# Kernel optimization log

Measured on AMD Instinct MI355X. Metric: run time of the kernel, lower is better.

The kernel has to match this reference:

```python
import jax, jax.numpy as jnp
import numpy as np

B, S, E, H = 1, 2048, 512, 8
D = E // H
N = B * S
WIN_HALF = 32  # attention_window 64 -> +/-32
ALPHA = 0.1
LN_EPS = 1e-12
NEG_INF = -1e9


def _build_window_edges():
    # windowed graph: dst i attends to src j with |i-j| <= WIN_HALF, within each batch block
    i = np.arange(S)
    offs = np.arange(-WIN_HALF, WIN_HALF + 1)
    src = i[:, None] + offs[None, :]
    dst = np.broadcast_to(i[:, None], src.shape)
    valid = (src >= 0) & (src < S)
    src, dst = src[valid], dst[valid]
    srcs, dsts = [], []
    for b in range(B):
        srcs.append(src + b * S)
        dsts.append(dst + b * S)
    return (np.concatenate(srcs).astype(np.int32),
            np.concatenate(dsts).astype(np.int32))


def setup_inputs() -> dict:
    key = jax.random.key(0)
    ks = jax.random.split(key, 12)
    sc = 1.0 / np.sqrt(E)
    src_np, dst_np = _build_window_edges()
    return {
        "hidden_states": jax.random.normal(ks[0], (B, S, E), dtype=jnp.float32),
        "attention_mask": jnp.zeros((B, S), dtype=jnp.float32),
        "edge_src": jnp.asarray(src_np),
        "edge_dst": jnp.asarray(dst_np),
        "Wq": jax.random.normal(ks[1], (E, E), dtype=jnp.float32) * sc,
        "bq": jnp.zeros((E,), dtype=jnp.float32),
        "Wk": jax.random.normal(ks[2], (E, E), dtype=jnp.float32) * sc,
        "bk": jnp.zeros((E,), dtype=jnp.float32),
        "Wv": jax.random.normal(ks[3], (E, E), dtype=jnp.float32) * sc,
        "bv": jnp.zeros((E,), dtype=jnp.float32),
        "Wo": jax.random.normal(ks[4], (E, E), dtype=jnp.float32) * sc,
        "bo": jnp.zeros((E,), dtype=jnp.float32),
        "ln_g": jnp.ones((E,), dtype=jnp.float32),
        "ln_b": jnp.zeros((E,), dtype=jnp.float32),
    }


def reference(hidden_states, attention_mask, edge_src, edge_dst,
              Wq, bq, Wk, bk, Wv, bv, Wo, bo, ln_g, ln_b):
    x = hidden_states  # (B,S,E); node ordering n = b*S + s (matches torch reshape)
    q = ((x @ Wq + bq) / jnp.sqrt(jnp.asarray(D, x.dtype))).reshape(N, H, D)
    k = (x @ Wk + bk).reshape(N, H, D)
    v = (x @ Wv + bv).reshape(N, H, D)

    mask = (attention_mask >= 0).reshape(N)  # bool per node

    # u_dot_v('k','q','score'): per-edge, per-head dot product
    score = jnp.einsum('ehd,ehd->eh', k[edge_src], q[edge_dst])  # (Eg,H)
    score = jnp.where(mask[edge_src][:, None], score, NEG_INF)

    # edge_softmax over incoming edges of each destination node
    smax = jax.ops.segment_max(score, edge_dst, num_segments=N)
    p = jnp.exp(score - smax[edge_dst])
    denom = jax.ops.segment_sum(p, edge_dst, num_segments=N)
    p = p / denom[edge_dst]  # (Eg,H)

    # 5 diffusion steps: h <- A h, blended with residual v (dropout off in eval)
    h = v
    for _ in range(5):
        m = h[edge_src] * p[:, :, None]                      # u_mul_e
        h = jax.ops.segment_sum(m, edge_dst, num_segments=N)  # sum('m','h')
        h = (1.0 - ALPHA) * h + ALPHA * v

    attn = h.reshape(B, S, E)

    # DiffuserSelfOutput: dense -> residual add -> LayerNorm
    y = attn @ Wo + bo + hidden_states
    mu = y.mean(-1, keepdims=True)
    var = ((y - mu) ** 2).mean(-1, keepdims=True)
    out = (y - mu) * jax.lax.rsqrt(var + LN_EPS) * ln_g + ln_b
    return out
```

## Files before the change

kernel.cpp:

```cpp
#include <hip/hip_runtime.h>
#include <math.h>

#define S_LEN 2048
#define E_DIM 512
#define NE (S_LEN * E_DIM)
#define H_NUM 8
#define WH 32
#define NOFF 65
#define PROW (H_NUM * NOFF)
#define PN (S_LEN * PROW)

typedef float f32x4 __attribute__((ext_vector_type(4)));
typedef short short8 __attribute__((ext_vector_type(8)));

__device__ __forceinline__ unsigned short f2bf(float f) {
    union { float f; unsigned u; } cv; cv.f = f;
    unsigned u = cv.u;
    u += 0x7fffu + ((u >> 16) & 1u);
    return (unsigned short)(u >> 16);
}
__device__ __forceinline__ unsigned pk2(float x, float y) {
    return (unsigned)f2bf(x) | ((unsigned)f2bf(y) << 16);
}

__device__ __forceinline__ void mfma_gemm_f32(
    const float* __restrict__ A, const float* __restrict__ W,
    const float* __restrict__ bias, float* __restrict__ C,
    float scale, int m0, int n0)
{
    __shared__ unsigned short As[64 * 40];
    __shared__ unsigned short Bs[64 * 40];
    const int tid = threadIdx.x;
    const int lane = tid & 63, wave = tid >> 6;
    const int quad = lane >> 4, l16 = lane & 15;
    const int wr = (wave >> 1) * 32, wc = (wave & 1) * 32;
    const int ar = tid >> 2, ac = (tid & 3) * 8;
    const int bn = tid & 63, bk0 = (tid >> 6) * 8;

    f32x4 acc00 = {0.f,0.f,0.f,0.f}, acc01 = acc00, acc10 = acc00, acc11 = acc00;

    for (int kk = 0; kk < E_DIM; kk += 32) {
        float4 a0 = *(const float4*)(A + (size_t)(m0 + ar) * E_DIM + kk + ac);
        float4 a1 = *(const float4*)(A + (size_t)(m0 + ar) * E_DIM + kk + ac + 4);
        float b[8];
#pragma unroll
        for (int j = 0; j < 8; ++j)
            b[j] = W[(size_t)(kk + bk0 + j) * E_DIM + n0 + bn];
        __syncthreads();
        uint4 ap; ap.x = pk2(a0.x, a0.y); ap.y = pk2(a0.z, a0.w);
        ap.z = pk2(a1.x, a1.y); ap.w = pk2(a1.z, a1.w);
        *(uint4*)(As + ar * 40 + ac) = ap;
        uint4 bp; bp.x = pk2(b[0], b[1]); bp.y = pk2(b[2], b[3]);
        bp.z = pk2(b[4], b[5]); bp.w = pk2(b[6], b[7]);
        *(uint4*)(Bs + bn * 40 + bk0) = bp;
        __syncthreads();
        short8 fa0 = *(const short8*)(As + (wr + l16) * 40 + quad * 8);
        short8 fa1 = *(const short8*)(As + (wr + 16 + l16) * 40 + quad * 8);
        short8 fb0 = *(const short8*)(Bs + (wc + l16) * 40 + quad * 8);
        short8 fb1 = *(const short8*)(Bs + (wc + 16 + l16) * 40 + quad * 8);
        acc00 = __builtin_amdgcn_mfma_f32_16x16x32_bf16(fa0, fb0, acc00, 0, 0, 0);
        acc01 = __builtin_amdgcn_mfma_f32_16x16x32_bf16(fa0, fb1, acc01, 0, 0, 0);
        acc10 = __builtin_amdgcn_mfma_f32_16x16x32_bf16(fa1, fb0, acc10, 0, 0, 0);
        acc11 = __builtin_amdgcn_mfma_f32_16x16x32_bf16(fa1, fb1, acc11, 0, 0, 0);
    }

#pragma unroll
    for (int mi = 0; mi < 2; ++mi) {
#pragma unroll
        for (int ni = 0; ni < 2; ++ni) {
            f32x4 a = (mi == 0) ? ((ni == 0) ? acc00 : acc01)
                                : ((ni == 0) ? acc10 : acc11);
            int n = n0 + wc + ni * 16 + l16;
            float bval = bias[n];
#pragma unroll
            for (int r = 0; r < 4; ++r) {
                int m = m0 + wr + mi * 16 + quad * 4 + r;
                C[(size_t)m * E_DIM + n] = (a[r] + bval) * scale;
            }
        }
    }
}

__global__ __launch_bounds__(256)
void qkv_gemm(const float* __restrict__ x,
              const float* __restrict__ Wq, const float* __restrict__ bq,
              const float* __restrict__ Wk, const float* __restrict__ bk,
              const float* __restrict__ Wv, const float* __restrict__ bv,
              float* __restrict__ q, float* __restrict__ k, float* __restrict__ v)
{
    const float* W; const float* b; float* o; float sc;
    if (blockIdx.z == 0)      { W = Wq; b = bq; o = q; sc = 0.125f; }
    else if (blockIdx.z == 1) { W = Wk; b = bk; o = k; sc = 1.0f; }
    else                      { W = Wv; b = bv; o = v; sc = 1.0f; }
    mfma_gemm_f32(x, W, b, o, sc, blockIdx.y * 64, blockIdx.x * 64);
}

#define SDN 32
__global__ __launch_bounds__(256)
void scores_kernel(const float* __restrict__ q, const float* __restrict__ k,
                   const float* __restrict__ amask, float* __restrict__ P)
{
    const int i0 = blockIdx.x * SDN;
    const int h  = blockIdx.y;
    const int tid = threadIdx.x;
    __shared__ float ks[96 * 68];
    __shared__ float am[96];
    __shared__ float sc[SDN * 66];
    __shared__ float smx[SDN], sidn[SDN];

    for (int e = tid; e < 96 * 16; e += 256) {
        int lr = e >> 4, c4 = e & 15;
        int j = i0 - WH + lr;
        int jc = min(max(j, 0), S_LEN - 1);
        *(float4*)(ks + lr * 68 + c4 * 4) =
            *(const float4*)(k + (size_t)jc * E_DIM + h * 64 + c4 * 4);
    }
    if (tid < 96) {
        int j = i0 - WH + tid;
        am[tid] = (j >= 0 && j < S_LEN) ? amask[j] : -1.0f;
    }

    const int dst = tid >> 3;
    const int og  = tid & 7;
    float4 qreg[16];
    {
        const float4* qrow = (const float4*)(q + (size_t)(i0 + dst) * E_DIM + h * 64);
#pragma unroll
        for (int t = 0; t < 16; ++t) qreg[t] = qrow[t];
    }
    __syncthreads();

    for (int off = og; off < NOFF; off += 8) {
        int j = i0 + dst + off - WH;
        float s;
        if (j < 0 || j >= S_LEN) {
            s = -INFINITY;
        } else {
            int lr = dst + off;
            const float4* kr = (const float4*)(ks + lr * 68);
            float acc = 0.f;
#pragma unroll
            for (int t = 0; t < 16; ++t) {
                float4 a = qreg[t], bb = kr[t];
                acc += a.x * bb.x + a.y * bb.y + a.z * bb.z + a.w * bb.w;
            }
            s = (am[lr] >= 0.f) ? acc : -1e9f;
        }
        sc[dst * 66 + off] = s;
    }
    __syncthreads();

    if (tid < SDN) {
        float mx = -INFINITY;
        for (int o = 0; o < NOFF; ++o) mx = fmaxf(mx, sc[tid * 66 + o]);
        float dn = 0.f;
        for (int o = 0; o < NOFF; ++o) dn += expf(sc[tid * 66 + o] - mx);
        smx[tid] = mx; sidn[tid] = 1.f / dn;
    }
    __syncthreads();

    for (int e = tid; e < SDN * NOFF; e += 256) {
        int d = e / NOFF, off = e - d * NOFF;
        float pv = expf(sc[d * 66 + off] - smx[d]) * sidn[d];
        P[(size_t)(i0 + d) * PROW + h * NOFF + off] = pv;
    }
}

__global__ __launch_bounds__(512)
void diffuse2(const float* __restrict__ hin, const float* __restrict__ v,
              const float* __restrict__ P, float* __restrict__ hout)
{
    const int i0 = blockIdx.x * 64;
    const int h  = blockIdx.y;
    const int tid = threadIdx.x;
    __shared__ float hs[192 * 64];
    __shared__ float h1[128 * 64];
    __shared__ float ps[128 * NOFF];

    for (int e = tid; e < 192 * 16; e += 512) {
        int lr = e >> 4, c4 = e & 15;
        int j = i0 - 64 + lr;
        int jc = min(max(j, 0), S_LEN - 1);
        *(float4*)(hs + lr * 64 + c4 * 4) =
            *(const float4*)(hin + (size_t)jc * E_DIM + h * 64 + c4 * 4);
    }
    for (int e = tid; e < 128 * NOFF; e += 512) {
        int mr = e / NOFF, o = e - mr * NOFF;
        int j = i0 - 32 + mr;
        int jc = min(max(j, 0), S_LEN - 1);
        ps[e] = P[(size_t)jc * PROW + h * NOFF + o];
    }
    __syncthreads();

    const int c4 = (tid & 15) * 4;
    const int g  = tid >> 4;
    const float4* h4 = (const float4*)hs;
    const int ci = tid & 15;

    {
        float4 a0 = {0,0,0,0}, a1 = a0, a2 = a0, a3 = a0;
        const int mb = g * 4;
        for (int lr = mb; lr < mb + 68; ++lr) {
            float4 hval = h4[lr * 16 + ci];
            int o0 = lr - mb;
            if ((unsigned)o0 <= 64u) {
                float p = ps[(mb + 0) * NOFF + o0];
                a0.x += p * hval.x; a0.y += p * hval.y; a0.z += p * hval.z; a0.w += p * hval.w;
            }
            int o1 = o0 - 1;
            if ((unsigned)o1 <= 64u) {
                float p = ps[(mb + 1) * NOFF + o1];
                a1.x += p * hval.x; a1.y += p * hval.y; a1.z += p * hval.z; a1.w += p * hval.w;
            }
            int o2 = o0 - 2;
            if ((unsigned)o2 <= 64u) {
                float p = ps[(mb + 2) * NOFF + o2];
                a2.x += p * hval.x; a2.y += p * hval.y; a2.z += p * hval.z; a2.w += p * hval.w;
            }
            int o3 = o0 - 3;
            if ((unsigned)o3 <= 64u) {
                float p = ps[(mb + 3) * NOFF + o3];
                a3.x += p * hval.x; a3.y += p * hval.y; a3.z += p * hval.z; a3.w += p * hval.w;
            }
        }
#pragma unroll
        for (int r = 0; r < 4; ++r) {
            float4 a = (r == 0) ? a0 : (r == 1) ? a1 : (r == 2) ? a2 : a3;
            int j = i0 - 32 + mb + r;
            int jc = min(max(j, 0), S_LEN - 1);
            float4 vv = *(const float4*)(v + (size_t)jc * E_DIM + h * 64 + c4);
            float4 o;
            o.x = 0.9f * a.x + 0.1f * vv.x;
            o.y = 0.9f * a.y + 0.1f * vv.y;
            o.z = 0.9f * a.z + 0.1f * vv.z;
            o.w = 0.9f * a.w + 0.1f * vv.w;
            *(float4*)(h1 + (mb + r) * 64 + c4) = o;
        }
    }
    __syncthreads();

    {
        const int ob = g * 2;
        const float4* m4 = (const float4*)h1;
        float4 a0 = {0,0,0,0}, a1 = a0;
        for (int lr = ob; lr < ob + 66; ++lr) {
            float4 hval = m4[lr * 16 + ci];
            int o0 = lr - ob;
            if ((unsigned)o0 <= 64u) {
                float p = ps[(ob + 32) * NOFF + o0];
                a0.x += p * hval.x; a0.y += p * hval.y; a0.z += p * hval.z; a0.w += p * hval.w;
            }
            int o1 = o0 - 1;
            if ((unsigned)o1 <= 64u) {
                float p = ps[(ob + 33) * NOFF + o1];
                a1.x += p * hval.x; a1.y += p * hval.y; a1.z += p * hval.z; a1.w += p * hval.w;
            }
        }
#pragma unroll
        for (int r = 0; r < 2; ++r) {
            float4 a = (r == 0) ? a0 : a1;
            size_t base = (size_t)(i0 + ob + r) * E_DIM + h * 64 + c4;
            float4 vv = *(const float4*)(v + base);
            float4 o;
            o.x = 0.9f * a.x + 0.1f * vv.x;
            o.y = 0.9f * a.y + 0.1f * vv.y;
            o.z = 0.9f * a.z + 0.1f * vv.z;
            o.w = 0.9f * a.w + 0.1f * vv.w;
            *(float4*)(hout + base) = o;
        }
    }
}

__global__ __launch_bounds__(256)
void diffuse1(const float* __restrict__ hin, const float* __restrict__ v,
              const float* __restrict__ P, float* __restrict__ hout)
{
    const int i0 = blockIdx.x * 32;
    const int h  = blockIdx.y;
    const int tid = threadIdx.x;
    __shared__ float hs[96 * 64];
    __shared__ float ps[32 * NOFF];

    for (int e = tid; e < 96 * 16; e += 256) {
        int lr = e >> 4, c4 = e & 15;
        int j = i0 - WH + lr;
        int jc = min(max(j, 0), S_LEN - 1);
        *(float4*)(hs + lr * 64 + c4 * 4) =
            *(const float4*)(hin + (size_t)jc * E_DIM + h * 64 + c4 * 4);
    }
    for (int e = tid; e < 32 * NOFF; e += 256) {
        int mr = e / NOFF, o = e - mr * NOFF;
        ps[e] = P[(size_t)(i0 + mr) * PROW + h * NOFF + o];
    }
    __syncthreads();

    const int c4 = (tid & 15) * 4;
    const int ci = tid & 15;
    const int g  = tid >> 4;
    const int ob = g * 2;
    const float4* h4 = (const float4*)hs;

    float4 a0 = {0,0,0,0}, a1 = a0;
    for (int lr = ob; lr < ob + 66; ++lr) {
        float4 hval = h4[lr * 16 + ci];
        int o0 = lr - ob;
        if ((unsigned)o0 <= 64u) {
            float p = ps[(ob + 0) * NOFF + o0];
            a0.x += p * hval.x; a0.y += p * hval.y; a0.z += p * hval.z; a0.w += p * hval.w;
        }
        int o1 = o0 - 1;
        if ((unsigned)o1 <= 64u) {
            float p = ps[(ob + 1) * NOFF + o1];
            a1.x += p * hval.x; a1.y += p * hval.y; a1.z += p * hval.z; a1.w += p * hval.w;
        }
    }
#pragma unroll
    for (int r = 0; r < 2; ++r) {
        float4 a = (r == 0) ? a0 : a1;
        size_t base = (size_t)(i0 + ob + r) * E_DIM + h * 64 + c4;
        float4 vv = *(const float4*)(v + base);
        float4 o;
        o.x = 0.9f * a.x + 0.1f * vv.x;
        o.y = 0.9f * a.y + 0.1f * vv.y;
        o.z = 0.9f * a.z + 0.1f * vv.z;
        o.w = 0.9f * a.w + 0.1f * vv.w;
        *(float4*)(hout + base) = o;
    }
}

__global__ __launch_bounds__(512)
void oln(const float* __restrict__ hsrc, const float* __restrict__ Wo,
         const float* __restrict__ bo, const float* __restrict__ x,
         const float* __restrict__ g, const float* __restrict__ lb,
         float* __restrict__ out)
{
    __shared__ unsigned short As[16 * 40];
    __shared__ unsigned short Bs[512 * 40];
    __shared__ float rsum[8][16], rsq[8][16];
    const int tid = threadIdx.x;
    const int lane = tid & 63, wave = tid >> 6;
    const int quad = lane >> 4, l16 = lane & 15;
    const int m0 = blockIdx.x * 16;
    const int n = tid;

    f32x4 acc[4];
#pragma unroll
    for (int t = 0; t < 4; ++t) acc[t] = (f32x4){0.f,0.f,0.f,0.f};

    for (int kk = 0; kk < E_DIM; kk += 32) {
        float4 av;
        if (tid < 128)
            av = *(const float4*)(hsrc + (size_t)(m0 + (tid >> 3)) * E_DIM + kk + (tid & 7) * 4);
        float bcol[32];
#pragma unroll
        for (int j = 0; j < 32; ++j)
            bcol[j] = Wo[(size_t)(kk + j) * E_DIM + n];
        __syncthreads();
        if (tid < 128) {
            uint2 ap; ap.x = pk2(av.x, av.y); ap.y = pk2(av.z, av.w);
            *(uint2*)(As + (tid >> 3) * 40 + (tid & 7) * 4) = ap;
        }
#pragma unroll
        for (int t = 0; t < 4; ++t) {
            uint4 bp;
            bp.x = pk2(bcol[t*8+0], bcol[t*8+1]); bp.y = pk2(bcol[t*8+2], bcol[t*8+3]);
            bp.z = pk2(bcol[t*8+4], bcol[t*8+5]); bp.w = pk2(bcol[t*8+6], bcol[t*8+7]);
            *(uint4*)(Bs + n * 40 + t * 8) = bp;
        }
        __syncthreads();
        short8 fa = *(const short8*)(As + l16 * 40 + quad * 8);
#pragma unroll
        for (int nt = 0; nt < 4; ++nt) {
            short8 fb = *(const short8*)(Bs + (wave * 64 + nt * 16 + l16) * 40 + quad * 8);
            acc[nt] = __builtin_amdgcn_mfma_f32_16x16x32_bf16(fa, fb, acc[nt], 0, 0, 0);
        }
    }

    float s[4] = {0.f,0.f,0.f,0.f}, s2[4] = {0.f,0.f,0.f,0.f};
#pragma unroll
    for (int nt = 0; nt < 4; ++nt) {
        int nc = wave * 64 + nt * 16 + l16;
        float bv = bo[nc];
#pragma unroll
        for (int r = 0; r < 4; ++r) {
            int m = m0 + quad * 4 + r;
            float vl = acc[nt][r] + bv + x[(size_t)m * E_DIM + nc];
            acc[nt][r] = vl;
            s[r] += vl; s2[r] += vl * vl;
        }
    }
#pragma unroll
    for (int o = 1; o < 16; o <<= 1) {
#pragma unroll
        for (int r = 0; r < 4; ++r) {
            s[r]  += __shfl_xor(s[r], o, 64);
            s2[r] += __shfl_xor(s2[r], o, 64);
        }
    }
    if (l16 == 0) {
#pragma unroll
        for (int r = 0; r < 4; ++r) {
            rsum[wave][quad * 4 + r] = s[r];
            rsq[wave][quad * 4 + r]  = s2[r];
        }
    }
    __syncthreads();
    float mu[4], rs[4];
#pragma unroll
    for (int r = 0; r < 4; ++r) {
        int rl = quad * 4 + r;
        float tot = 0.f, tot2 = 0.f;
#pragma unroll
        for (int w = 0; w < 8; ++w) { tot += rsum[w][rl]; tot2 += rsq[w][rl]; }
        float m_ = tot * (1.f / 512.f);
        float var = tot2 * (1.f / 512.f) - m_ * m_;
        mu[r] = m_; rs[r] = rsqrtf(var + 1e-12f);
    }
#pragma unroll
    for (int nt = 0; nt < 4; ++nt) {
        int nc = wave * 64 + nt * 16 + l16;
        float gv = g[nc], bbv = lb[nc];
#pragma unroll
        for (int r = 0; r < 4; ++r) {
            int m = m0 + quad * 4 + r;
            out[(size_t)m * E_DIM + nc] = (acc[nt][r] - mu[r]) * rs[r] * gv + bbv;
        }
    }
}

extern "C" void kernel_launch(void* const* d_in, const int* in_sizes, int n_in,
                              void* d_out, int out_size, void* d_ws, size_t ws_size,
                              hipStream_t stream)
{
    const float* x     = (const float*)d_in[0];
    const float* amask = (const float*)d_in[1];
    const float* Wq = (const float*)d_in[4];
    const float* bq = (const float*)d_in[5];
    const float* Wk = (const float*)d_in[6];
    const float* bk = (const float*)d_in[7];
    const float* Wv = (const float*)d_in[8];
    const float* bv = (const float*)d_in[9];
    const float* Wo = (const float*)d_in[10];
    const float* bo = (const float*)d_in[11];
    const float* lng = (const float*)d_in[12];
    const float* lnb = (const float*)d_in[13];
    float* out = (float*)d_out;

    float* ws = (float*)d_ws;
    float* q  = ws;
    float* k  = ws + (size_t)NE;
    float* v  = ws + (size_t)2 * NE;
    float* P  = ws + (size_t)3 * NE;
    float* hA = ws + (size_t)3 * NE + PN;
    float* hB = hA + (size_t)NE;

    qkv_gemm<<<dim3(8, 32, 3), 256, 0, stream>>>(x, Wq, bq, Wk, bk, Wv, bv, q, k, v);

    scores_kernel<<<dim3(64, 8), 256, 0, stream>>>(q, k, amask, P);

    diffuse2<<<dim3(32, 8), 512, 0, stream>>>(v,  v, P, hA);
    diffuse2<<<dim3(32, 8), 512, 0, stream>>>(hA, v, P, hB);
    diffuse1<<<dim3(64, 8), 256, 0, stream>>>(hB, v, P, hA);

    oln<<<128, 512, 0, stream>>>(hA, Wo, bo, x, lng, lnb, out);
}
```

Before: 183.7 us.

## Fuse final diffusion step into output GEMM and halve diffuse2 channel tiles

The fifth diffusion step is folded into the output projection and LayerNorm kernel: each 32-wide K slice computes the windowed aggregation of hB for its 16 rows in shared memory and feeds the bf16 A tile straight into the MFMA. This removes one kernel launch and the round trip of the final h through global memory. The two-step diffusion kernel now handles 32 channels per block instead of a whole head, giving twice as many blocks and padded shared rows. The cost is redundant reads of an 80-row halo in the GEMM kernel, extra barriers per K step, and a scalar aggregation loop on the GEMM's critical path.

```diff
diff --git a/kernel.cpp b/kernel.cpp
--- a/kernel.cpp
+++ b/kernel.cpp
@@ -167,22 +167,23 @@
 }
 
 __global__ __launch_bounds__(512)
-void diffuse2(const float* __restrict__ hin, const float* __restrict__ v,
-              const float* __restrict__ P, float* __restrict__ hout)
+void diffuse2c(const float* __restrict__ hin, const float* __restrict__ v,
+               const float* __restrict__ P, float* __restrict__ hout)
 {
     const int i0 = blockIdx.x * 64;
-    const int h  = blockIdx.y;
+    const int c0 = blockIdx.y * 32;
+    const int h  = c0 >> 6;
     const int tid = threadIdx.x;
-    __shared__ float hs[192 * 64];
-    __shared__ float h1[128 * 64];
+    __shared__ float hs[192 * 36];
+    __shared__ float h1[128 * 36];
     __shared__ float ps[128 * NOFF];
 
-    for (int e = tid; e < 192 * 16; e += 512) {
-        int lr = e >> 4, c4 = e & 15;
+    for (int e = tid; e < 192 * 8; e += 512) {
+        int lr = e >> 3, c4 = e & 7;
         int j = i0 - 64 + lr;
         int jc = min(max(j, 0), S_LEN - 1);
-        *(float4*)(hs + lr * 64 + c4 * 4) =
-            *(const float4*)(hin + (size_t)jc * E_DIM + h * 64 + c4 * 4);
+        *(float4*)(hs + lr * 36 + c4 * 4) =
+            *(const float4*)(hin + (size_t)jc * E_DIM + c0 + c4 * 4);
     }
     for (int e = tid; e < 128 * NOFF; e += 512) {
         int mr = e / NOFF, o = e - mr * NOFF;
@@ -192,132 +193,48 @@
     }
     __syncthreads();
 
-    const int c4 = (tid & 15) * 4;
-    const int g  = tid >> 4;
-    const float4* h4 = (const float4*)hs;
-    const int ci = tid & 15;
+    const int ci = tid & 7;
+    const int g  = tid >> 3;
 
     {
-        float4 a0 = {0,0,0,0}, a1 = a0, a2 = a0, a3 = a0;
-        const int mb = g * 4;
-        for (int lr = mb; lr < mb + 68; ++lr) {
-            float4 hval = h4[lr * 16 + ci];
-            int o0 = lr - mb;
-            if ((unsigned)o0 <= 64u) {
-                float p = ps[(mb + 0) * NOFF + o0];
+        float4 a0 = {0,0,0,0}, a1 = a0;
+        const int mb = g * 2;
+        for (int lr = 0; lr < 66; ++lr) {
+            float4 hval = *(const float4*)(hs + (mb + lr) * 36 + ci * 4);
+            if (lr <= 64) {
+                float p = ps[mb * NOFF + lr];
                 a0.x += p * hval.x; a0.y += p * hval.y; a0.z += p * hval.z; a0.w += p * hval.w;
             }
-            int o1 = o0 - 1;
+            int o1 = lr - 1;
             if ((unsigned)o1 <= 64u) {
                 float p = ps[(mb + 1) * NOFF + o1];
                 a1.x += p * hval.x; a1.y += p * hval.y; a1.z += p * hval.z; a1.w += p * hval.w;
             }
-            int o2 = o0 - 2;
-            if ((unsigned)o2 <= 64u) {
-                float p = ps[(mb + 2) * NOFF + o2];
-                a2.x += p * hval.x; a2.y += p * hval.y; a2.z += p * hval.z; a2.w += p * hval.w;
-            }
-            int o3 = o0 - 3;
-            if ((unsigned)o3 <= 64u) {
-                float p = ps[(mb + 3) * NOFF + o3];
-                a3.x += p * hval.x; a3.y += p * hval.y; a3.z += p * hval.z; a3.w += p * hval.w;
-            }
-        }
-#pragma unroll
-        for (int r = 0; r < 4; ++r) {
-            float4 a = (r == 0) ? a0 : (r == 1) ? a1 : (r == 2) ? a2 : a3;
+        }
+#pragma unroll
+        for (int r = 0; r < 2; ++r) {
+            float4 a = r ? a1 : a0;
             int j = i0 - 32 + mb + r;
             int jc = min(max(j, 0), S_LEN - 1);
-            float4 vv = *(const float4*)(v + (size_t)jc * E_DIM + h * 64 + c4);
+            float4 vv = *(const float4*)(v + (size_t)jc * E_DIM + c0 + ci * 4);
             float4 o;
             o.x = 0.9f * a.x + 0.1f * vv.x;
             o.y = 0.9f * a.y + 0.1f * vv.y;
             o.z = 0.9f * a.z + 0.1f * vv.z;
             o.w = 0.9f * a.w + 0.1f * vv.w;
-            *(float4*)(h1 + (mb + r) * 64 + c4) = o;
+            *(float4*)(h1 + (mb + r) * 36 + ci * 4) = o;
         }
     }
     __syncthreads();
 
     {
-        const int ob = g * 2;
-        const float4* m4 = (const float4*)h1;
-        float4 a0 = {0,0,0,0}, a1 = a0;
-        for (int lr = ob; lr < ob + 66; ++lr) {
-            float4 hval = m4[lr * 16 + ci];
-            int o0 = lr - ob;
-            if ((unsigned)o0 <= 64u) {
-                float p = ps[(ob + 32) * NOFF + o0];
-                a0.x += p * hval.x; a0.y += p * hval.y; a0.z += p * hval.z; a0.w += p * hval.w;
-            }
-            int o1 = o0 - 1;
-            if ((unsigned)o1 <= 64u) {
-                float p = ps[(ob + 33) * NOFF + o1];
-                a1.x += p * hval.x; a1.y += p * hval.y; a1.z += p * hval.z; a1.w += p * hval.w;
-            }
-        }
-#pragma unroll
-        for (int r = 0; r < 2; ++r) {
-            float4 a = (r == 0) ? a0 : a1;
-            size_t base = (size_t)(i0 + ob + r) * E_DIM + h * 64 + c4;
-            float4 vv = *(const float4*)(v + base);
-            float4 o;
-            o.x = 0.9f * a.x + 0.1f * vv.x;
-            o.y = 0.9f * a.y + 0.1f * vv.y;
-            o.z = 0.9f * a.z + 0.1f * vv.z;
-            o.w = 0.9f * a.w + 0.1f * vv.w;
-            *(float4*)(hout + base) = o;
-        }
-    }
-}
-
-__global__ __launch_bounds__(256)
-void diffuse1(const float* __restrict__ hin, const float* __restrict__ v,
-              const float* __restrict__ P, float* __restrict__ hout)
-{
-    const int i0 = blockIdx.x * 32;
-    const int h  = blockIdx.y;
-    const int tid = threadIdx.x;
-    __shared__ float hs[96 * 64];
-    __shared__ float ps[32 * NOFF];
-
-    for (int e = tid; e < 96 * 16; e += 256) {
-        int lr = e >> 4, c4 = e & 15;
-        int j = i0 - WH + lr;
-        int jc = min(max(j, 0), S_LEN - 1);
-        *(float4*)(hs + lr * 64 + c4 * 4) =
-            *(const float4*)(hin + (size_t)jc * E_DIM + h * 64 + c4 * 4);
-    }
-    for (int e = tid; e < 32 * NOFF; e += 256) {
-        int mr = e / NOFF, o = e - mr * NOFF;
-        ps[e] = P[(size_t)(i0 + mr) * PROW + h * NOFF + o];
-    }
-    __syncthreads();
-
-    const int c4 = (tid & 15) * 4;
-    const int ci = tid & 15;
-    const int g  = tid >> 4;
-    const int ob = g * 2;
-    const float4* h4 = (const float4*)hs;
-
-    float4 a0 = {0,0,0,0}, a1 = a0;
-    for (int lr = ob; lr < ob + 66; ++lr) {
-        float4 hval = h4[lr * 16 + ci];
-        int o0 = lr - ob;
-        if ((unsigned)o0 <= 64u) {
-            float p = ps[(ob + 0) * NOFF + o0];
-            a0.x += p * hval.x; a0.y += p * hval.y; a0.z += p * hval.z; a0.w += p * hval.w;
-        }
-        int o1 = o0 - 1;
-        if ((unsigned)o1 <= 64u) {
-            float p = ps[(ob + 1) * NOFF + o1];
-            a1.x += p * hval.x; a1.y += p * hval.y; a1.z += p * hval.z; a1.w += p * hval.w;
-        }
-    }
-#pragma unroll
-    for (int r = 0; r < 2; ++r) {
-        float4 a = (r == 0) ? a0 : a1;
-        size_t base = (size_t)(i0 + ob + r) * E_DIM + h * 64 + c4;
+        float4 a = {0,0,0,0};
+        for (int off = 0; off < NOFF; ++off) {
+            float4 hval = *(const float4*)(h1 + (g + off) * 36 + ci * 4);
+            float p = ps[(g + 32) * NOFF + off];
+            a.x += p * hval.x; a.y += p * hval.y; a.z += p * hval.z; a.w += p * hval.w;
+        }
+        size_t base = (size_t)(i0 + g) * E_DIM + c0 + ci * 4;
         float4 vv = *(const float4*)(v + base);
         float4 o;
         o.x = 0.9f * a.x + 0.1f * vv.x;
@@ -329,13 +246,17 @@
 }
 
 __global__ __launch_bounds__(512)
-void oln(const float* __restrict__ hsrc, const float* __restrict__ Wo,
-         const float* __restrict__ bo, const float* __restrict__ x,
-         const float* __restrict__ g, const float* __restrict__ lb,
-         float* __restrict__ out)
+void oln2(const float* __restrict__ hB, const float* __restrict__ v,
+          const float* __restrict__ P, const float* __restrict__ Wo,
+          const float* __restrict__ bo, const float* __restrict__ x,
+          const float* __restrict__ g, const float* __restrict__ lb,
+          float* __restrict__ out)
 {
     __shared__ unsigned short As[16 * 40];
     __shared__ unsigned short Bs[512 * 40];
+    __shared__ float hBs[80 * 37];
+    __shared__ float Ps[16 * PROW];
+    __shared__ float vs[16 * 32];
     __shared__ float rsum[8][16], rsq[8][16];
     const int tid = threadIdx.x;
     const int lane = tid & 63, wave = tid >> 6;
@@ -343,23 +264,48 @@
     const int m0 = blockIdx.x * 16;
     const int n = tid;
 
+    for (int e = tid; e < 16 * PROW; e += 512)
+        Ps[e] = P[(size_t)(m0 + e / PROW) * PROW + (e % PROW)];
+
     f32x4 acc[4];
 #pragma unroll
     for (int t = 0; t < 4; ++t) acc[t] = (f32x4){0.f,0.f,0.f,0.f};
 
     for (int kk = 0; kk < E_DIM; kk += 32) {
-        float4 av;
+        const int hd = kk >> 6;
+        float4 hv4;
+        {
+            int lr = tid >> 3, c4 = tid & 7;
+            int j = m0 - 32 + lr;
+            int jc = min(max(j, 0), S_LEN - 1);
+            hv4 = *(const float4*)(hB + (size_t)jc * E_DIM + kk + c4 * 4);
+        }
+        float4 hv4b;
+        if (tid < 128) {
+            int lr = 64 + (tid >> 3), c4 = tid & 7;
+            int j = m0 - 32 + lr;
+            int jc = min(max(j, 0), S_LEN - 1);
+            hv4b = *(const float4*)(hB + (size_t)jc * E_DIM + kk + c4 * 4);
+        }
+        float4 vv4;
         if (tid < 128)
-            av = *(const float4*)(hsrc + (size_t)(m0 + (tid >> 3)) * E_DIM + kk + (tid & 7) * 4);
+            vv4 = *(const float4*)(v + (size_t)(m0 + (tid >> 3)) * E_DIM + kk + (tid & 7) * 4);
         float bcol[32];
 #pragma unroll
         for (int j = 0; j < 32; ++j)
             bcol[j] = Wo[(size_t)(kk + j) * E_DIM + n];
+
         __syncthreads();
+        {
+            int lr = tid >> 3, c4 = tid & 7;
+            *(float4*)(hBs + lr * 37 + c4 * 4) = hv4;
+        }
         if (tid < 128) {
-            uint2 ap; ap.x = pk2(av.x, av.y); ap.y = pk2(av.z, av.w);
-            *(uint2*)(As + (tid >> 3) * 40 + (tid & 7) * 4) = ap;
-        }
+            int lr = 64 + (tid >> 3), c4 = tid & 7;
+            *(float4*)(hBs + lr * 37 + c4 * 4) = hv4b;
+        }
+        if (tid < 128)
+            *(float4*)(vs + (tid >> 3) * 32 + (tid & 7) * 4) = vv4;
 #pragma unroll
         for (int t = 0; t < 4; ++t) {
             uint4 bp;
@@ -368,6 +314,22 @@
             *(uint4*)(Bs + n * 40 + t * 8) = bp;
         }
         __syncthreads();
+
+        if (tid < 256) {
+            int r = tid >> 4, cp = (tid & 15) * 2;
+            const float* pr = Ps + r * PROW + hd * NOFF;
+            float a0 = 0.f, a1 = 0.f;
+            for (int off = 0; off < NOFF; ++off) {
+                float p = pr[off];
+                a0 += p * hBs[(r + off) * 37 + cp];
+                a1 += p * hBs[(r + off) * 37 + cp + 1];
+            }
+            float h0 = 0.9f * a0 + 0.1f * vs[r * 32 + cp];
+            float h1 = 0.9f * a1 + 0.1f * vs[r * 32 + cp + 1];
+            *(unsigned*)(As + r * 40 + cp) = pk2(h0, h1);
+        }
+        __syncthreads();
+
         short8 fa = *(const short8*)(As + l16 * 40 + quad * 8);
 #pragma unroll
         for (int nt = 0; nt < 4; ++nt) {
@@ -458,9 +420,8 @@
 
     scores_kernel<<<dim3(64, 8), 256, 0, stream>>>(q, k, amask, P);
 
-    diffuse2<<<dim3(32, 8), 512, 0, stream>>>(v,  v, P, hA);
-    diffuse2<<<dim3(32, 8), 512, 0, stream>>>(hA, v, P, hB);
-    diffuse1<<<dim3(64, 8), 256, 0, stream>>>(hB, v, P, hA);
-
-    oln<<<128, 512, 0, stream>>>(hA, Wo, bo, x, lng, lnb, out);
-}
+    diffuse2c<<<dim3(32, 16), 512, 0, stream>>>(v,  v, P, hA);
+    diffuse2c<<<dim3(32, 16), 512, 0, stream>>>(hA, v, P, hB);
+
+    oln2<<<128, 512, 0, stream>>>(hB, v, P, Wo, bo, x, lng, lnb, out);
+}
```

Measured after the change: 186.2 us. Within noise of the previous version (+1.4%).
